# Performance work log

Hardware: AMD Instinct MI355X
Metric: run time of the kernel (lower is better)

## Reference

```python
import jax, jax.numpy as jnp
import numpy as np
from jax.scipy.linalg import solve_triangular

EMB = 2048; NKH = 16; NVH = 32; DK = 128; DV = 128
KSZ = 4; EPS = 1e-6; CHUNK = 64
KEY_DIM = NKH * DK; VAL_DIM = NVH * DV
CONV_DIM = 2 * KEY_DIM + VAL_DIM  # q,k (key_dim each) + v (value_dim)
B, S = 1, 4096  # S % CHUNK == 0 -> no padding path


def setup_inputs() -> dict:
    key = jax.random.key(0)
    ks = jax.random.split(key, 7)
    s = 0.02
    return {
        "hidden_states": jax.random.normal(ks[0], (B, S, EMB), jnp.float32),
        "W_qkvz": jax.random.normal(ks[1], (EMB, 2 * KEY_DIM + 2 * VAL_DIM), jnp.float32) * s,
        "W_ba": jax.random.normal(ks[2], (EMB, 2 * NVH), jnp.float32) * s,
        "conv_kernel": jax.random.normal(ks[3], (KSZ, 1, CONV_DIM), jnp.float32) * 0.1,
        "A_log": jnp.log(jax.random.uniform(ks[4], (NVH,), jnp.float32, 1e-9, 16.0)),
        "dt_bias": jnp.ones((NVH,), jnp.float32),
        "norm_weight": jnp.ones((DV,), jnp.float32),
        "W_out": jax.random.normal(ks[5], (VAL_DIM, EMB), jnp.float32) * s,
    }


def _chunk_gated_delta_rule(q, k, v, g, beta):
    """q,k: [B,S,H,DK]; v: [B,S,H,DV]; g,beta: [B,S,H]. Returns [B,S,H,DV]."""
    dt = q.dtype
    prec = jax.lax.Precision.HIGHEST
    q = jnp.transpose(q, (0, 2, 1, 3)).astype(jnp.float32)
    k = jnp.transpose(k, (0, 2, 1, 3)).astype(jnp.float32)
    v = jnp.transpose(v, (0, 2, 1, 3)).astype(jnp.float32)
    beta = jnp.transpose(beta, (0, 2, 1)).astype(jnp.float32)
    g = jnp.transpose(g, (0, 2, 1)).astype(jnp.float32)
    b, h, s, dk = k.shape
    dv = v.shape[-1]
    nc = s // CHUNK
    q = q * jax.lax.rsqrt(jnp.float32(dk))
    v_beta = v * beta[..., None]
    k_beta = k * beta[..., None]
    qc = q.reshape(b, h, nc, CHUNK, dk)
    kc = k.reshape(b, h, nc, CHUNK, dk)
    kbc = k_beta.reshape(b, h, nc, CHUNK, dk)
    vbc = v_beta.reshape(b, h, nc, CHUNK, dv)
    gc = g.reshape(b, h, nc, CHUNK)
    g_cum = jnp.cumsum(gc, axis=-1)                        # [b,h,nc,C]
    g_diff = g_cum[..., :, None] - g_cum[..., None, :]     # [b,h,nc,C,C]
    decay = jnp.exp(jnp.tril(g_diff))
    tri_incl = jnp.triu(jnp.ones((CHUNK, CHUNK), bool), k=0)
    L = -jnp.matmul(kbc, jnp.swapaxes(kc, -1, -2), precision=prec) * decay
    L = jnp.where(tri_incl, 0.0, L)  # strictly lower
    eye = jnp.eye(CHUNK, dtype=jnp.float32)
    # UT transform: original fori_loop forward-substitution == (I - L)^{-1}
    attn = solve_triangular(eye - L, jnp.broadcast_to(eye, L.shape), lower=True)
    v_intra = jnp.matmul(attn, vbc, precision=prec)
    k_cumdecay = jnp.matmul(attn, kbc * jnp.exp(g_cum)[..., None], precision=prec)
    state0 = jnp.zeros((b, h, dk, dv), jnp.float32)
    tri_strict = jnp.triu(jnp.ones((CHUNK, CHUNK), bool), k=1)
    xs = tuple(jnp.moveaxis(t, 2, 0) for t in (qc, kc, v_intra, k_cumdecay, g_cum, decay))

    def scan_body(state, x):
        q_i, k_i, v_i, kcd_i, g_i, dm_i = x
        a_i = jnp.matmul(q_i, jnp.swapaxes(k_i, -1, -2), precision=prec) * dm_i
        a_i = jnp.where(tri_strict, 0.0, a_i)
        v_new = v_i - jnp.matmul(kcd_i, state, precision=prec)
        out_i = jnp.matmul(q_i * jnp.exp(g_i)[..., None], state, precision=prec) \
              + jnp.matmul(a_i, v_new, precision=prec)
        g_last = g_i[..., -1]
        new_state = state * jnp.exp(g_last)[..., None, None] \
            + jnp.matmul(jnp.swapaxes(k_i * jnp.exp(g_last[..., None] - g_i)[..., None], -1, -2),
                         v_new, precision=prec)
        return new_state, out_i

    _, out = jax.lax.scan(scan_body, state0, xs)
    out = jnp.moveaxis(out, 0, 2).reshape(b, h, s, dv)
    return jnp.transpose(out, (0, 2, 1, 3)).astype(dt)


def reference(hidden_states, W_qkvz, W_ba, conv_kernel, A_log, dt_bias, norm_weight, W_out):
    b, s, _ = hidden_states.shape
    vk = NVH // NKH  # v heads per k head
    qkvz = hidden_states @ W_qkvz                          # [b,s,12288]
    ba = hidden_states @ W_ba                              # [b,s,64]
    mixed = qkvz.reshape(b, s, NKH, 2 * DK + 2 * vk * DV)
    q, k, v_raw, z_raw = jnp.split(mixed, [DK, 2 * DK, 2 * DK + vk * DV], axis=3)
    value = v_raw.reshape(b, s, NVH, DV)
    z = z_raw.reshape(b, s, NVH, DV)
    mixed_ba = ba.reshape(b, s, NKH, 2 * vk)
    b_raw, a_raw = jnp.split(mixed_ba, [vk], axis=3)
    b_gate = b_raw.reshape(b, s, NVH)
    a_gate = a_raw.reshape(b, s, NVH)
    # depthwise causal conv over the concatenated q,k,v channels
    qkv = jnp.concatenate([q.reshape(b, s, -1), k.reshape(b, s, -1), value.reshape(b, s, -1)], axis=-1)
    x = jnp.pad(qkv, ((0, 0), (KSZ - 1, 0), (0, 0)))
    conv = jax.lax.conv_general_dilated(x, conv_kernel, (1,), 'VALID',
                                        dimension_numbers=('NWC', 'WIO', 'NWC'),
                                        feature_group_count=CONV_DIM)
    qkv_c = jax.nn.silu(conv.astype(jnp.float32)).astype(hidden_states.dtype)
    q_c, k_c, v_c = jnp.split(qkv_c, [KEY_DIM, 2 * KEY_DIM], axis=-1)
    query = q_c.reshape(b, s, NKH, DK)
    key = k_c.reshape(b, s, NKH, DK)
    value = v_c.reshape(b, s, NVH, DV)
    beta = jax.nn.sigmoid(b_gate)
    g = (-jnp.exp(A_log.astype(jnp.float32))
         * jax.nn.softplus(a_gate.astype(jnp.float32) + dt_bias.astype(jnp.float32))
         ).astype(hidden_states.dtype)
    query = jnp.repeat(query, vk, axis=2)
    key = jnp.repeat(key, vk, axis=2)
    core = _chunk_gated_delta_rule(query, key, value, g, beta)  # [b,s,NVH,DV]
    # gated RMSNorm (Mamba2-style): gate first, then normalize
    xf = core.astype(jnp.float32) * jax.nn.silu(z.astype(jnp.float32))
    var = jnp.mean(xf * xf, axis=-1, keepdims=True)
    xf = xf * jax.lax.rsqrt(var + EPS) * norm_weight
    out = xf.astype(hidden_states.dtype).reshape(b, s, VAL_DIM)
    return out @ W_out
```

## Files before the change

kernel.cpp:

```cpp
#include <hip/hip_runtime.h>


typedef __attribute__((ext_vector_type(8))) __bf16 bf16x8;
typedef __attribute__((ext_vector_type(4))) float f32x4;
typedef __bf16 bf16_t;

#define MFMA_BF16(A, B, C) __builtin_amdgcn_mfma_f32_16x16x32_bf16((A), (B), (C), 0, 0, 0)

__device__ __forceinline__ void async16(const bf16_t* g, bf16_t* l) {
  __builtin_amdgcn_global_load_lds(
      (const __attribute__((address_space(1))) unsigned*)g,
      (__attribute__((address_space(3))) unsigned*)l, 16, 0, 0);
}

__device__ __forceinline__ bf16_t f2bf(float x) {
  unsigned u = __builtin_bit_cast(unsigned, x);
  unsigned r = u + 0x7fffu + ((u >> 16) & 1u);
  unsigned short s = (unsigned short)(r >> 16);
  return __builtin_bit_cast(bf16_t, s);
}
__device__ __forceinline__ float bf2f(bf16_t b) {
  unsigned short s = __builtin_bit_cast(unsigned short, b);
  unsigned u = ((unsigned)s) << 16;
  return __builtin_bit_cast(float, u);
}
__device__ __forceinline__ unsigned packhl(float x) {
  bf16_t h = f2bf(x);
  bf16_t l = f2bf(x - bf2f(h));
  return (((unsigned)__builtin_bit_cast(unsigned short, h)) << 16) |
         (unsigned)__builtin_bit_cast(unsigned short, l);
}
__device__ __forceinline__ float upk(unsigned u) {
  return __builtin_bit_cast(float, u & 0xffff0000u) +
         __builtin_bit_cast(float, u << 16);
}

struct FragPair { bf16x8 hi, lo; };

__device__ __forceinline__ void load8(float v[8], const float* p) {
  float4 a = *(const float4*)p;
  float4 b = *(const float4*)(p + 4);
  v[0] = a.x; v[1] = a.y; v[2] = a.z; v[3] = a.w;
  v[4] = b.x; v[5] = b.y; v[6] = b.z; v[7] = b.w;
}
__device__ __forceinline__ void load8u(unsigned v[8], const unsigned* p) {
  uint4 a = *(const uint4*)p;
  uint4 b = *(const uint4*)(p + 4);
  v[0] = a.x; v[1] = a.y; v[2] = a.z; v[3] = a.w;
  v[4] = b.x; v[5] = b.y; v[6] = b.z; v[7] = b.w;
}
__device__ __forceinline__ FragPair split8(const float v[8]) {
  FragPair f;
#pragma unroll
  for (int j = 0; j < 8; j++) {
    bf16_t h = f2bf(v[j]);
    f.hi[j] = h;
    f.lo[j] = f2bf(v[j] - bf2f(h));
  }
  return f;
}
__device__ __forceinline__ FragPair unpack8(const unsigned v[8]) {
  FragPair f;
#pragma unroll
  for (int j = 0; j < 8; j++) {
    f.hi[j] = __builtin_bit_cast(bf16_t, (unsigned short)(v[j] >> 16));
    f.lo[j] = __builtin_bit_cast(bf16_t, (unsigned short)(v[j] & 0xffffu));
  }
  return f;
}
__device__ __forceinline__ f32x4 mfma3(const FragPair& A, const FragPair& B, f32x4 c) {
  c = MFMA_BF16(A.hi, B.hi, c);
  c = MFMA_BF16(A.hi, B.lo, c);
  c = MFMA_BF16(A.lo, B.hi, c);
  return c;
}

__global__ void k_cvt(const float* __restrict__ in, bf16_t* __restrict__ out, int n) {
  int i = (blockIdx.x * 256 + threadIdx.x) * 4;
  if (i + 3 < n) {
    float4 v = *(const float4*)(in + i);
    out[i + 0] = f2bf(v.x); out[i + 1] = f2bf(v.y);
    out[i + 2] = f2bf(v.z); out[i + 3] = f2bf(v.w);
  }
}

__global__ void k_transpose_cvt(const float* __restrict__ in, bf16_t* __restrict__ out,
                                int K, int N) {
  __shared__ bf16_t tile[64 * 65];
  int n0 = blockIdx.x * 64, k0 = blockIdx.y * 64;
  int c = threadIdx.x & 63, rg = threadIdx.x >> 6;
#pragma unroll
  for (int rr = 0; rr < 16; rr++) {
    int r = rr * 4 + rg;
    tile[c * 65 + r] = f2bf(in[(size_t)(k0 + r) * N + n0 + c]);
  }
  __syncthreads();
#pragma unroll
  for (int rr = 0; rr < 16; rr++) {
    int r = rr * 4 + rg;
    out[(size_t)(n0 + r) * K + k0 + c] = tile[r * 65 + c];
  }
}

__global__ void k_ktrans(const bf16_t* __restrict__ kb, bf16_t* __restrict__ kbT) {
  __shared__ __align__(16) bf16_t t[128][72];
  int kh = blockIdx.x >> 6, ci = blockIdx.x & 63, s0 = ci * 64;
  int s = threadIdx.x & 63, dg = threadIdx.x >> 6;
  const bf16_t* src = kb + (size_t)(s0 + s) * 2048 + kh * 128 + dg * 32;
#pragma unroll
  for (int j = 0; j < 4; j++) {
    bf16x8 v = *(const bf16x8*)(src + j * 8);
#pragma unroll
    for (int e = 0; e < 8; e++) t[dg * 32 + j * 8 + e][s] = v[e];
  }
  __syncthreads();
  int d = threadIdx.x >> 1, sh = (threadIdx.x & 1) * 32;
  bf16_t* dst = kbT + ((size_t)blockIdx.x * 128 + d) * 64 + sh;
#pragma unroll
  for (int j = 0; j < 4; j++)
    *(bf16x8*)(dst + j * 8) = *(const bf16x8*)(&t[d][sh + j * 8]);
}

__global__ __launch_bounds__(256) void k_gemm(const bf16_t* __restrict__ A,
                                              const bf16_t* __restrict__ BT,
                                              float* __restrict__ C, int M, int N, int K) {
  __shared__ __align__(16) bf16_t sA[128 * 32];
  __shared__ __align__(16) bf16_t sB[128 * 32];
  const int tid = threadIdx.x;
  const int lane = tid & 63, w = tid >> 6;
  const int quad = lane >> 4, l15 = lane & 15;
  const int m0 = blockIdx.y * 128, n0 = blockIdx.x * 128;
  const int wm = (w >> 1) * 64, wn = (w & 1) * 64;
  f32x4 acc[4][4];
#pragma unroll
  for (int a = 0; a < 4; a++)
#pragma unroll
    for (int b = 0; b < 4; b++) { f32x4 z = {0.f, 0.f, 0.f, 0.f}; acc[a][b] = z; }
  const int sb = (lane & 7) ^ ((lane >> 3) & 7);
  const int srow = ((tid >> 3) << 1) + (sb >> 2);
  const int scol = (sb & 3) * 8;
  const bf16_t* gA = A + (size_t)(m0 + srow) * K + scol;
  const bf16_t* gB = BT + (size_t)(n0 + srow) * K + scol;
  bf16_t* lA = sA + w * 512;
  bf16_t* lB = sB + w * 512;
  const int rh = l15 >> 1;
  const int bs = (((l15 & 1) << 2) + quad) ^ rh;
  const int foff = rh * 64 + bs * 8;
  for (int kt = 0; kt < K; kt += 32) {
    async16(gA + kt, lA);
    async16(gA + (size_t)64 * K + kt, lA + 2048);
    async16(gB + kt, lB);
    async16(gB + (size_t)64 * K + kt, lB + 2048);
    __syncthreads();
    bf16x8 af[4], bfv[4];
#pragma unroll
    for (int t = 0; t < 4; t++) {
      af[t]  = *(const bf16x8*)(sA + ((wm >> 1) + t * 8) * 64 + foff);
      bfv[t] = *(const bf16x8*)(sB + ((wn >> 1) + t * 8) * 64 + foff);
    }
#pragma unroll
    for (int mt = 0; mt < 4; mt++)
#pragma unroll
      for (int nt = 0; nt < 4; nt++)
        acc[mt][nt] = MFMA_BF16(af[mt], bfv[nt], acc[mt][nt]);
    __syncthreads();
  }
#pragma unroll
  for (int mt = 0; mt < 4; mt++)
#pragma unroll
    for (int nt = 0; nt < 4; nt++) {
      int row0 = m0 + wm + mt * 16 + quad * 4;
      int col = n0 + wn + nt * 16 + l15;
#pragma unroll
      for (int r = 0; r < 4; r++)
        C[(size_t)(row0 + r) * N + col] = acc[mt][nt][r];
    }
}

__global__ __launch_bounds__(256) void k_gemm_qkvz(const bf16_t* __restrict__ A,
                                                   const bf16_t* __restrict__ BT,
                                                   bf16_t* __restrict__ qkvb,
                                                   bf16_t* __restrict__ zb,
                                                   int M, int N, int K) {
  __shared__ __align__(16) bf16_t sA[128 * 32];
  __shared__ __align__(16) bf16_t sB[128 * 32];
  const int tid = threadIdx.x;
  const int lane = tid & 63, w = tid >> 6;
  const int quad = lane >> 4, l15 = lane & 15;
  const int m0 = blockIdx.y * 128, n0 = blockIdx.x * 128;
  const int wm = (w >> 1) * 64, wn = (w & 1) * 64;
  f32x4 acc[4][4];
#pragma unroll
  for (int a = 0; a < 4; a++)
#pragma unroll
    for (int b = 0; b < 4; b++) { f32x4 z = {0.f, 0.f, 0.f, 0.f}; acc[a][b] = z; }
  const int sb = (lane & 7) ^ ((lane >> 3) & 7);
  const int srow = ((tid >> 3) << 1) + (sb >> 2);
  const int scol = (sb & 3) * 8;
  const bf16_t* gA = A + (size_t)(m0 + srow) * K + scol;
  const bf16_t* gB = BT + (size_t)(n0 + srow) * K + scol;
  bf16_t* lA = sA + w * 512;
  bf16_t* lB = sB + w * 512;
  const int rh = l15 >> 1;
  const int bs = (((l15 & 1) << 2) + quad) ^ rh;
  const int foff = rh * 64 + bs * 8;
  for (int kt = 0; kt < K; kt += 32) {
    async16(gA + kt, lA);
    async16(gA + (size_t)64 * K + kt, lA + 2048);
    async16(gB + kt, lB);
    async16(gB + (size_t)64 * K + kt, lB + 2048);
    __syncthreads();
    bf16x8 af[4], bfv[4];
#pragma unroll
    for (int t = 0; t < 4; t++) {
      af[t]  = *(const bf16x8*)(sA + ((wm >> 1) + t * 8) * 64 + foff);
      bfv[t] = *(const bf16x8*)(sB + ((wn >> 1) + t * 8) * 64 + foff);
    }
#pragma unroll
    for (int mt = 0; mt < 4; mt++)
#pragma unroll
      for (int nt = 0; nt < 4; nt++)
        acc[mt][nt] = MFMA_BF16(af[mt], bfv[nt], acc[mt][nt]);
    __syncthreads();
  }
#pragma unroll
  for (int nt = 0; nt < 4; nt++) {
    int c = n0 + wn + nt * 16 + l15;
    int kh = c / 768;
    int rr = c - kh * 768;
    bool isz = (rr >= 512);
    bf16_t* dst = isz ? zb : qkvb;
    size_t stride = isz ? 4096 : 8192;
    size_t coff = isz ? (size_t)(kh * 256 + (rr - 512)) : (size_t)(kh * 512 + rr);
#pragma unroll
    for (int mt = 0; mt < 4; mt++) {
      int row0 = m0 + wm + mt * 16 + quad * 4;
#pragma unroll
      for (int r = 0; r < 4; r++)
        dst[(size_t)(row0 + r) * stride + coff] = f2bf(acc[mt][nt][r]);
    }
  }
}

__global__ __launch_bounds__(256) void k_ba(const float* __restrict__ hs,
                                            const float* __restrict__ Wba,
                                            const float* __restrict__ A_log,
                                            const float* __restrict__ dtb,
                                            float* __restrict__ g, float* __restrict__ beta) {
  __shared__ float sH[4][2048];
  int s0 = blockIdx.x * 32;
  int c = threadIdx.x & 63, sg = threadIdx.x >> 6;
  for (int rg = 0; rg < 8; rg++) {
    __syncthreads();
    for (int i = threadIdx.x; i < 2048; i += 256) {
      int r = i >> 9, kk = (i & 511) * 4;
      *(float4*)(&sH[r][kk]) = *(const float4*)(hs + (size_t)(s0 + rg * 4 + r) * 2048 + kk);
    }
    __syncthreads();
    float dot = 0.f;
    for (int kk = 0; kk < 2048; kk += 4) {
      float4 hv = *(const float4*)(&sH[sg][kk]);
      dot += hv.x * Wba[(kk + 0) * 64 + c] + hv.y * Wba[(kk + 1) * 64 + c] +
             hv.z * Wba[(kk + 2) * 64 + c] + hv.w * Wba[(kk + 3) * 64 + c];
    }
    int s = s0 + rg * 4 + sg;
    int hh = c >> 2, j = c & 3;
    if (j < 2) {
      int vh = hh * 2 + j;
      beta[s * 32 + vh] = 1.f / (1.f + __expf(-dot));
    } else {
      int vh = hh * 2 + (j - 2);
      float x = dot + dtb[vh];
      float sp = (x > 20.f) ? x : log1pf(__expf(x));
      g[s * 32 + vh] = -__expf(A_log[vh]) * sp;
    }
  }
}

__global__ void k_conv(const bf16_t* __restrict__ qkvb, const float* __restrict__ ck,
                       bf16_t* __restrict__ qb, bf16_t* __restrict__ kb,
                       bf16_t* __restrict__ vb) {
  int c = blockIdx.x * 256 + threadIdx.x;
  int s0 = blockIdx.y * 128;
  int col, dstc, dstride;
  bf16_t* dst;
  float scale = 1.0f;
  if (c < 2048) {
    int hh = c >> 7, d = c & 127;
    col = hh * 512 + d; dst = qb; dstc = c; dstride = 2048;
    scale = 0.08838834764831845f;
  } else if (c < 4096) {
    int cc = c - 2048, hh = cc >> 7, d = cc & 127;
    col = hh * 512 + 128 + d; dst = kb; dstc = cc; dstride = 2048;
  } else {
    int cc = c - 4096, vh = cc >> 7, d = cc & 127;
    col = (vh >> 1) * 512 + 256 + (vh & 1) * 128 + d; dst = vb; dstc = cc; dstride = 4096;
  }
  float w0 = ck[c], w1 = ck[8192 + c], w2 = ck[2 * 8192 + c], w3 = ck[3 * 8192 + c];
  float x0 = 0.f, x1 = 0.f, x2 = 0.f;
  if (s0 >= 3) {
    x0 = bf2f(qkvb[(size_t)(s0 - 3) * 8192 + col]);
    x1 = bf2f(qkvb[(size_t)(s0 - 2) * 8192 + col]);
    x2 = bf2f(qkvb[(size_t)(s0 - 1) * 8192 + col]);
  }
  for (int s = s0; s < s0 + 128; s++) {
    float x3 = bf2f(qkvb[(size_t)s * 8192 + col]);
    float y = w0 * x0 + w1 * x1 + w2 * x2 + w3 * x3;
    y = y / (1.f + __expf(-y));
    dst[(size_t)s * dstride + dstc] = f2bf(y * scale);
    x0 = x1; x1 = x2; x2 = x3;
  }
}

__global__ __launch_bounds__(256) void k_phaseA(const bf16_t* __restrict__ kb,
                                                const bf16_t* __restrict__ vb,
                                                const float* __restrict__ g,
                                                const float* __restrict__ beta,
                                                float* __restrict__ vi,
                                                bf16_t* __restrict__ kcdn) {
  __shared__ __align__(16) char smem[36608];
  float* sGc = (float*)smem;
  float* sBt = (float*)(smem + 256);
  float* sBE = (float*)(smem + 512);
  float* sP  = (float*)(smem + 768);
  bf16_t* sQ  = (bf16_t*)(smem + 18176);
  bf16_t* sQT = (bf16_t*)(smem + 27392);
  bf16_t* sVT = (bf16_t*)(smem + 18176);
  bf16_t* sKT = (bf16_t*)(smem + 27392);

  const int tid = threadIdx.x, lane = tid & 63, w = tid >> 6;
  const int quad = lane >> 4, l15 = lane & 15;
  const int h = blockIdx.x >> 6, ci = blockIdx.x & 63;
  const int kh = h >> 1, s0 = ci * 64;
  const int m = w * 16 + l15;

  if (tid < 64) {
    float gv = g[(size_t)(s0 + tid) * 32 + h];
    float bv = beta[(size_t)(s0 + tid) * 32 + h];
#pragma unroll
    for (int off = 1; off < 64; off <<= 1) {
      float t = __shfl_up(gv, off, 64);
      if (tid >= off) gv += t;
    }
    sGc[tid] = gv; sBt[tid] = bv; sBE[tid] = bv * __expf(gv);
  }
  __syncthreads();

  const bf16_t* krow = kb + (size_t)s0 * 2048 + kh * 128;
  bf16x8 ak[4];
#pragma unroll
  for (int ks = 0; ks < 4; ks++)
    ak[ks] = *(const bf16x8*)(krow + (size_t)m * 2048 + ks * 32 + quad * 8);
  f32x4 accL[4];
#pragma unroll
  for (int nt = 0; nt < 4; nt++) { f32x4 z = {0.f, 0.f, 0.f, 0.f}; accL[nt] = z; }
#pragma unroll
  for (int nt = 0; nt < 4; nt++)
#pragma unroll
    for (int ks = 0; ks < 4; ks++) {
      bf16x8 bk = *(const bf16x8*)(krow + (size_t)(nt * 16 + l15) * 2048 + ks * 32 + quad * 8);
      accL[nt] = MFMA_BF16(ak[ks], bk, accL[nt]);
    }
#pragma unroll
  for (int nt = 0; nt < 4; nt++) {
    int j = nt * 16 + l15;
#pragma unroll
    for (int r = 0; r < 4; r++) {
      int i = w * 16 + quad * 4 + r;
      float Lij = (i > j) ? (-accL[nt][r] * sBt[i] * __expf(sGc[i] - sGc[j])) : 0.f;
      sP[i * 68 + j] = ((i == j) ? 1.f : 0.f) + Lij;
      bf16_t q16 = f2bf(Lij);
      sQ[i * 72 + j] = q16;
      sQT[j * 72 + i] = q16;
    }
  }
  __syncthreads();

  for (int it = 0; it < 5; it++) {
    f32x4 accQ[4];
#pragma unroll
    for (int nt = 0; nt < 4; nt++) { f32x4 z = {0.f, 0.f, 0.f, 0.f}; accQ[nt] = z; }
    bf16x8 qa[2];
#pragma unroll
    for (int ks = 0; ks < 2; ks++)
      qa[ks] = *(const bf16x8*)(sQ + m * 72 + ks * 32 + quad * 8);
#pragma unroll
    for (int nt = 0; nt < 4; nt++)
#pragma unroll
      for (int ks = 0; ks < 2; ks++) {
        bf16x8 qv = *(const bf16x8*)(sQT + (nt * 16 + l15) * 72 + ks * 32 + quad * 8);
        accQ[nt] = MFMA_BF16(qa[ks], qv, accQ[nt]);
      }
    __syncthreads();
#pragma unroll
    for (int nt = 0; nt < 4; nt++) {
      int j = nt * 16 + l15;
#pragma unroll
      for (int r = 0; r < 4; r++) {
        int i = w * 16 + quad * 4 + r;
        bf16_t q16 = f2bf(accQ[nt][r]);
        sQ[i * 72 + j] = q16;
        sQT[j * 72 + i] = q16;
      }
    }
    __syncthreads();
    f32x4 accP[4];
#pragma unroll
    for (int nt = 0; nt < 4; nt++) { f32x4 z = {0.f, 0.f, 0.f, 0.f}; accP[nt] = z; }
    FragPair pa[2];
#pragma unroll
    for (int ks = 0; ks < 2; ks++) {
      float v[8];
      load8(v, sP + m * 68 + ks * 32 + quad * 8);
      pa[ks] = split8(v);
    }
#pragma unroll
    for (int nt = 0; nt < 4; nt++)
#pragma unroll
      for (int ks = 0; ks < 2; ks++) {
        bf16x8 qv = *(const bf16x8*)(sQT + (nt * 16 + l15) * 72 + ks * 32 + quad * 8);
        accP[nt] = MFMA_BF16(pa[ks].hi, qv, accP[nt]);
        accP[nt] = MFMA_BF16(pa[ks].lo, qv, accP[nt]);
      }
#pragma unroll
    for (int nt = 0; nt < 4; nt++) {
      int j = nt * 16 + l15;
#pragma unroll
      for (int r = 0; r < 4; r++) {
        int i = w * 16 + quad * 4 + r;
        sP[i * 68 + j] += accP[nt][r];
      }
    }
  }

  FragPair paV[2], paK[2];
#pragma unroll
  for (int ks = 0; ks < 2; ks++) {
    float v[8];
    load8(v, sP + m * 68 + ks * 32 + quad * 8);
    float vv[8], vk[8];
#pragma unroll
    for (int jj = 0; jj < 8; jj++) {
      int i = ks * 32 + quad * 8 + jj;
      vv[jj] = v[jj] * sBt[i];
      vk[jj] = v[jj] * sBE[i];
    }
    paV[ks] = split8(vv);
    paK[ks] = split8(vk);
  }

  for (int hf = 0; hf < 2; hf++) {
    __syncthreads();
    {
      int sidx = tid & 63, dg = tid >> 6;
      const bf16_t* vsrc = vb + (size_t)(s0 + sidx) * 4096 + h * 128 + hf * 64 + dg * 16;
      const bf16_t* ksrc = kb + (size_t)(s0 + sidx) * 2048 + kh * 128 + hf * 64 + dg * 16;
      bf16x8 v0 = *(const bf16x8*)vsrc;
      bf16x8 v1 = *(const bf16x8*)(vsrc + 8);
      bf16x8 k0 = *(const bf16x8*)ksrc;
      bf16x8 k1 = *(const bf16x8*)(ksrc + 8);
#pragma unroll
      for (int e = 0; e < 8; e++) {
        sVT[(dg * 16 + e) * 72 + sidx] = v0[e];
        sVT[(dg * 16 + 8 + e) * 72 + sidx] = v1[e];
        sKT[(dg * 16 + e) * 72 + sidx] = k0[e];
        sKT[(dg * 16 + 8 + e) * 72 + sidx] = k1[e];
      }
    }
    __syncthreads();
    f32x4 accV[4], accK[4];
#pragma unroll
    for (int nt = 0; nt < 4; nt++) {
      f32x4 z = {0.f, 0.f, 0.f, 0.f};
      accV[nt] = z; accK[nt] = z;
    }
#pragma unroll
    for (int nt = 0; nt < 4; nt++)
#pragma unroll
      for (int ks = 0; ks < 2; ks++) {
        bf16x8 bv = *(const bf16x8*)(sVT + (nt * 16 + l15) * 72 + ks * 32 + quad * 8);
        accV[nt] = MFMA_BF16(paV[ks].hi, bv, accV[nt]);
        accV[nt] = MFMA_BF16(paV[ks].lo, bv, accV[nt]);
        bf16x8 bk = *(const bf16x8*)(sKT + (nt * 16 + l15) * 72 + ks * 32 + quad * 8);
        accK[nt] = MFMA_BF16(paK[ks].hi, bk, accK[nt]);
        accK[nt] = MFMA_BF16(paK[ks].lo, bk, accK[nt]);
      }
#pragma unroll
    for (int nt = 0; nt < 4; nt++) {
      int col = hf * 64 + nt * 16 + l15;
#pragma unroll
      for (int r = 0; r < 4; r++) {
        int row = w * 16 + quad * 4 + r;
        size_t o = ((size_t)h * 4096 + s0 + row) * 128 + col;
        vi[o] = accV[nt][r];
        kcdn[o] = f2bf(-accK[nt][r]);
      }
    }
  }
}

__global__ __launch_bounds__(256) void k_phaseB(const bf16_t* __restrict__ qb,
                                                const bf16_t* __restrict__ kbT,
                                                const float* __restrict__ g,
                                                const float* __restrict__ vi,
                                                const bf16_t* __restrict__ kcdn,
                                                bf16_t* __restrict__ vnT,
                                                bf16_t* __restrict__ outp) {
  __shared__ __align__(16) char smem[13312];
  float* sGc2 = (float*)smem;
  unsigned* sSTp = (unsigned*)(smem + 512);
  unsigned* sVTp = (unsigned*)(smem + 8960);
  const int tid = threadIdx.x, lane = tid & 63, w = tid >> 6;
  const int quad = lane >> 4, l15 = lane & 15;
  const int h = blockIdx.x >> 3, cg = blockIdx.x & 7;
  const int kh = h >> 1, col0 = cg * 16;
  const int m = w * 16 + l15;

  for (int i = tid; i < 16 * 132; i += 256) sSTp[i] = 0u;
  if (tid < 64) {
    float gv = g[(size_t)tid * 32 + h];
#pragma unroll
    for (int off = 1; off < 64; off <<= 1) {
      float t = __shfl_up(gv, off, 64);
      if (tid >= off) gv += t;
    }
    sGc2[tid] = gv;
  }
  __syncthreads();

  for (int ci = 0; ci < 64; ci++) {
    const int s0 = ci * 64;
    const float* sGc = sGc2 + (ci & 1) * 64;

    const bf16_t* kcrow = kcdn + ((size_t)h * 4096 + s0 + m) * 128;
    const bf16_t* qrow = qb + (size_t)(s0 + m) * 2048 + kh * 128;
    bf16x8 a1[4], a2[4], kT[2][2];
#pragma unroll
    for (int d = 0; d < 4; d++) {
      a1[d] = *(const bf16x8*)(kcrow + d * 32 + quad * 8);
      a2[d] = *(const bf16x8*)(qrow + d * 32 + quad * 8);
    }
#pragma unroll
    for (int mi = 0; mi < 2; mi++)
#pragma unroll
      for (int ks = 0; ks < 2; ks++)
        kT[mi][ks] = *(const bf16x8*)(kbT + ((size_t)(kh * 64 + ci) * 128 +
                                             w * 32 + mi * 16 + l15) * 64 + ks * 32 + quad * 8);
    const int colg = col0 + l15;
    size_t vbase = ((size_t)h * 4096 + s0 + w * 16 + quad * 4) * 128 + colg;
    f32x4 accV = {vi[vbase], vi[vbase + 128], vi[vbase + 256], vi[vbase + 384]};
    f32x4 accO = {0.f, 0.f, 0.f, 0.f};
#pragma unroll
    for (int d = 0; d < 4; d++) {
      unsigned u[8];
      load8u(u, sSTp + l15 * 132 + d * 32 + quad * 8);
      FragPair B = unpack8(u);
      accV = MFMA_BF16(a1[d], B.hi, accV);
      accV = MFMA_BF16(a1[d], B.lo, accV);
      accO = MFMA_BF16(a2[d], B.hi, accO);
      accO = MFMA_BF16(a2[d], B.lo, accO);
    }
    const float gl = sGc[63];
    {
      bf16_t* vout = vnT + ((size_t)(h * 64 + ci) * 128 + colg) * 64 + w * 16 + quad * 4;
      bf16_t* oout = outp + vbase;
      ushort4 vv;
      unsigned pk[4];
      unsigned short vb_[4];
#pragma unroll
      for (int r = 0; r < 4; r++) {
        float gr = sGc[w * 16 + quad * 4 + r];
        oout[(size_t)r * 128] = f2bf(accO[r] * __expf(gr));
        vb_[r] = __builtin_bit_cast(unsigned short, f2bf(accV[r]));
        pk[r] = packhl(accV[r] * __expf(gl - gr));
      }
      vv.x = vb_[0]; vv.y = vb_[1]; vv.z = vb_[2]; vv.w = vb_[3];
      *(ushort4*)vout = vv;
      uint4 pv; pv.x = pk[0]; pv.y = pk[1]; pv.z = pk[2]; pv.w = pk[3];
      *(uint4*)(sVTp + l15 * 68 + w * 16 + quad * 4) = pv;
    }
    __syncthreads();

    f32x4 accD[2];
#pragma unroll
    for (int mi = 0; mi < 2; mi++) { f32x4 z = {0.f, 0.f, 0.f, 0.f}; accD[mi] = z; }
#pragma unroll
    for (int ks = 0; ks < 2; ks++) {
      unsigned u[8];
      load8u(u, sVTp + l15 * 68 + ks * 32 + quad * 8);
      FragPair Bv = unpack8(u);
#pragma unroll
      for (int mi = 0; mi < 2; mi++) {
        accD[mi] = MFMA_BF16(kT[mi][ks], Bv.hi, accD[mi]);
        accD[mi] = MFMA_BF16(kT[mi][ks], Bv.lo, accD[mi]);
      }
    }
    float egl = __expf(gl);
#pragma unroll
    for (int mi = 0; mi < 2; mi++) {
      int row0 = w * 32 + mi * 16 + quad * 4;
      unsigned* ps = sSTp + l15 * 132 + row0;
      uint4 old4 = *(uint4*)ps;
      uint4 nu;
      nu.x = packhl(upk(old4.x) * egl + accD[mi][0]);
      nu.y = packhl(upk(old4.y) * egl + accD[mi][1]);
      nu.z = packhl(upk(old4.z) * egl + accD[mi][2]);
      nu.w = packhl(upk(old4.w) * egl + accD[mi][3]);
      *(uint4*)ps = nu;
    }
    if (ci + 1 < 64 && tid < 64) {
      float gv = g[(size_t)((ci + 1) * 64 + tid) * 32 + h];
#pragma unroll
      for (int off = 1; off < 64; off <<= 1) {
        float t = __shfl_up(gv, off, 64);
        if (tid >= off) gv += t;
      }
      sGc2[((ci + 1) & 1) * 64 + tid] = gv;
    }
    __syncthreads();
  }
}

__global__ __launch_bounds__(256) void k_phaseC(const bf16_t* __restrict__ qb,
                                                const bf16_t* __restrict__ kb,
                                                const float* __restrict__ g,
                                                const bf16_t* __restrict__ vnT,
                                                const bf16_t* __restrict__ outp,
                                                const bf16_t* __restrict__ zb,
                                                const float* __restrict__ nw,
                                                bf16_t* __restrict__ xf) {
  __shared__ __align__(16) char smem[17664];
  float* sGc = (float*)smem;
  unsigned* sAp = (unsigned*)(smem + 256);
  const int tid = threadIdx.x, lane = tid & 63, w = tid >> 6;
  const int quad = lane >> 4, l15 = lane & 15;
  const int h = blockIdx.x >> 6, ci = blockIdx.x & 63;
  const int kh = h >> 1, s0 = ci * 64;
  const int m = w * 16 + l15;

  if (tid < 64) {
    float gv = g[(size_t)(s0 + tid) * 32 + h];
#pragma unroll
    for (int off = 1; off < 64; off <<= 1) {
      float t = __shfl_up(gv, off, 64);
      if (tid >= off) gv += t;
    }
    sGc[tid] = gv;
  }
  __syncthreads();

  const bf16_t* qrow = qb + (size_t)s0 * 2048 + kh * 128;
  const bf16_t* krow = kb + (size_t)s0 * 2048 + kh * 128;
  bf16x8 aq[4];
#pragma unroll
  for (int ks = 0; ks < 4; ks++)
    aq[ks] = *(const bf16x8*)(qrow + (size_t)m * 2048 + ks * 32 + quad * 8);
  f32x4 accA[4];
#pragma unroll
  for (int nt = 0; nt < 4; nt++) { f32x4 z = {0.f, 0.f, 0.f, 0.f}; accA[nt] = z; }
#pragma unroll
  for (int nt = 0; nt < 4; nt++)
#pragma unroll
    for (int ks = 0; ks < 4; ks++) {
      bf16x8 bk = *(const bf16x8*)(krow + (size_t)(nt * 16 + l15) * 2048 + ks * 32 + quad * 8);
      accA[nt] = MFMA_BF16(aq[ks], bk, accA[nt]);
    }
#pragma unroll
  for (int nt = 0; nt < 4; nt++) {
    int j = nt * 16 + l15;
#pragma unroll
    for (int r = 0; r < 4; r++) {
      int i = w * 16 + quad * 4 + r;
      float a = (i >= j) ? accA[nt][r] * __expf(sGc[i] - sGc[j]) : 0.f;
      sAp[i * 68 + j] = packhl(a);
    }
  }
  __syncthreads();

  FragPair Aa[2];
#pragma unroll
  for (int ks = 0; ks < 2; ks++) {
    unsigned u[8];
    load8u(u, sAp + m * 68 + ks * 32 + quad * 8);
    Aa[ks] = unpack8(u);
  }
  f32x4 accO[8];
#pragma unroll
  for (int nt = 0; nt < 8; nt++) {
    size_t base = ((size_t)h * 4096 + s0 + w * 16 + quad * 4) * 128 + nt * 16 + l15;
    f32x4 z;
    z[0] = bf2f(outp[base]); z[1] = bf2f(outp[base + 128]);
    z[2] = bf2f(outp[base + 256]); z[3] = bf2f(outp[base + 384]);
    accO[nt] = z;
  }
#pragma unroll
  for (int nt = 0; nt < 8; nt++)
#pragma unroll
    for (int ks = 0; ks < 2; ks++) {
      bf16x8 bv = *(const bf16x8*)(vnT + ((size_t)(h * 64 + ci) * 128 + nt * 16 + l15) * 64 +
                                   ks * 32 + quad * 8);
      accO[nt] = MFMA_BF16(Aa[ks].hi, bv, accO[nt]);
      accO[nt] = MFMA_BF16(Aa[ks].lo, bv, accO[nt]);
    }

  float xv[8][4];
  float ss[4] = {0.f, 0.f, 0.f, 0.f};
#pragma unroll
  for (int nt = 0; nt < 8; nt++) {
    int dv = nt * 16 + l15;
#pragma unroll
    for (int r = 0; r < 4; r++) {
      int s = s0 + w * 16 + quad * 4 + r;
      float z = bf2f(zb[(size_t)s * 4096 + h * 128 + dv]);
      float gate = z / (1.f + __expf(-z));
      float val = accO[nt][r] * gate;
      xv[nt][r] = val;
      ss[r] += val * val;
    }
  }
#pragma unroll
  for (int off = 1; off < 16; off <<= 1) {
#pragma unroll
    for (int r = 0; r < 4; r++) ss[r] += __shfl_xor(ss[r], off, 64);
  }
  float rs[4];
#pragma unroll
  for (int r = 0; r < 4; r++) rs[r] = rsqrtf(ss[r] * (1.f / 128.f) + 1e-6f);
#pragma unroll
  for (int nt = 0; nt < 8; nt++) {
    int dv = nt * 16 + l15;
    float nwv = nw[dv];
#pragma unroll
    for (int r = 0; r < 4; r++) {
      int s = s0 + w * 16 + quad * 4 + r;
      xf[(size_t)s * 4096 + h * 128 + dv] = f2bf(xv[nt][r] * rs[r] * nwv);
    }
  }
}

extern "C" void kernel_launch(void* const* d_in, const int* in_sizes, int n_in,
                              void* d_out, int out_size, void* d_ws, size_t ws_size,
                              hipStream_t stream) {
  const float* hs = (const float*)d_in[0];
  const float* Wqkvz = (const float*)d_in[1];
  const float* Wba = (const float*)d_in[2];
  const float* convk = (const float*)d_in[3];
  const float* A_log = (const float*)d_in[4];
  const float* dtb = (const float*)d_in[5];
  const float* nw = (const float*)d_in[6];
  const float* Wout = (const float*)d_in[7];
  float* out = (float*)d_out;
  char* ws = (char*)d_ws;

  const size_t NEED = 252706816u;
  if (ws_size < NEED) return;

  bf16_t* hsbf = (bf16_t*)(ws + 0);
  bf16_t* wqkT = (bf16_t*)(ws + 16777216);
  bf16_t* qb   = (bf16_t*)(ws + 0);
  bf16_t* kb   = (bf16_t*)(ws + 16777216);
  bf16_t* vb   = (bf16_t*)(ws + 33554432);
  bf16_t* vnT  = (bf16_t*)(ws + 33554432);
  bf16_t* qkvb = (bf16_t*)(ws + 67108864);
  float*  vi   = (float*)(ws + 67108864);
  bf16_t* xf   = (bf16_t*)(ws + 67108864);
  bf16_t* zb   = (bf16_t*)(ws + 134217728);
  float*  gbuf = (float*)(ws + 167772160);
  float*  bbuf = (float*)(ws + 168296448);
  bf16_t* kcdn = (bf16_t*)(ws + 168820736);
  bf16_t* woutT= (bf16_t*)(ws + 168820736);
  bf16_t* outp = (bf16_t*)(ws + 202375168);
  bf16_t* kbT  = (bf16_t*)(ws + 235929600);

  k_cvt<<<8192, 256, 0, stream>>>(hs, hsbf, 4096 * 2048);
  k_transpose_cvt<<<dim3(192, 32), 256, 0, stream>>>(Wqkvz, wqkT, 2048, 12288);
  k_gemm_qkvz<<<dim3(96, 32), 256, 0, stream>>>(hsbf, wqkT, qkvb, zb,
                                                4096, 12288, 2048);
  k_ba<<<128, 256, 0, stream>>>(hs, Wba, A_log, dtb, gbuf, bbuf);
  k_conv<<<dim3(32, 32), 256, 0, stream>>>(qkvb, convk, qb, kb, vb);
  k_ktrans<<<1024, 256, 0, stream>>>(kb, kbT);
  k_phaseA<<<2048, 256, 0, stream>>>(kb, vb, gbuf, bbuf, vi, kcdn);
  k_phaseB<<<256, 256, 0, stream>>>(qb, kbT, gbuf, vi, kcdn, vnT, outp);
  k_phaseC<<<2048, 256, 0, stream>>>(qb, kb, gbuf, vnT, outp, zb, nw, xf);
  k_transpose_cvt<<<dim3(32, 64), 256, 0, stream>>>(Wout, woutT, 4096, 2048);
  k_gemm<<<dim3(16, 32), 256, 0, stream>>>(xf, woutT, out, 4096, 2048, 4096);
}
```

Before: 1.096 ms.

## Rewrite QKVZ GEMM with 256x256 tiles, 4-stage async LDS pipeline, XCD swizzle

After: 1.094 ms. About the same (-0.2%).

```diff
diff --git a/kernel.cpp b/kernel.cpp
--- a/kernel.cpp
+++ b/kernel.cpp
@@ -67,12 +67,6 @@
     f.lo[j] = __builtin_bit_cast(bf16_t, (unsigned short)(v[j] & 0xffffu));
   }
   return f;
-}
-__device__ __forceinline__ f32x4 mfma3(const FragPair& A, const FragPair& B, f32x4 c) {
-  c = MFMA_BF16(A.hi, B.hi, c);
-  c = MFMA_BF16(A.hi, B.lo, c);
-  c = MFMA_BF16(A.lo, B.hi, c);
-  return c;
 }
 
 __global__ void k_cvt(const float* __restrict__ in, bf16_t* __restrict__ out, int n) {
@@ -177,55 +171,93 @@
     }
 }
 
-__global__ __launch_bounds__(256) void k_gemm_qkvz(const bf16_t* __restrict__ A,
-                                                   const bf16_t* __restrict__ BT,
-                                                   bf16_t* __restrict__ qkvb,
-                                                   bf16_t* __restrict__ zb,
-                                                   int M, int N, int K) {
-  __shared__ __align__(16) bf16_t sA[128 * 32];
-  __shared__ __align__(16) bf16_t sB[128 * 32];
+__global__ __launch_bounds__(512, 2) void k_gemm_qkvz(const bf16_t* __restrict__ A,
+                                                      const bf16_t* __restrict__ BT,
+                                                      bf16_t* __restrict__ qkvb,
+                                                      bf16_t* __restrict__ zb,
+                                                      int M, int N, int K) {
+  __shared__ __align__(16) bf16_t sA[4 * 8192];
+  __shared__ __align__(16) bf16_t sB[4 * 8192];
   const int tid = threadIdx.x;
   const int lane = tid & 63, w = tid >> 6;
   const int quad = lane >> 4, l15 = lane & 15;
-  const int m0 = blockIdx.y * 128, n0 = blockIdx.x * 128;
-  const int wm = (w >> 1) * 64, wn = (w & 1) * 64;
-  f32x4 acc[4][4];
-#pragma unroll
-  for (int a = 0; a < 4; a++)
-#pragma unroll
-    for (int b = 0; b < 4; b++) { f32x4 z = {0.f, 0.f, 0.f, 0.f}; acc[a][b] = z; }
-  const int sb = (lane & 7) ^ ((lane >> 3) & 7);
-  const int srow = ((tid >> 3) << 1) + (sb >> 2);
-  const int scol = (sb & 3) * 8;
-  const bf16_t* gA = A + (size_t)(m0 + srow) * K + scol;
-  const bf16_t* gB = BT + (size_t)(n0 + srow) * K + scol;
-  bf16_t* lA = sA + w * 512;
-  bf16_t* lB = sB + w * 512;
-  const int rh = l15 >> 1;
-  const int bs = (((l15 & 1) << 2) + quad) ^ rh;
-  const int foff = rh * 64 + bs * 8;
-  for (int kt = 0; kt < K; kt += 32) {
-    async16(gA + kt, lA);
-    async16(gA + (size_t)64 * K + kt, lA + 2048);
-    async16(gB + kt, lB);
-    async16(gB + (size_t)64 * K + kt, lB + 2048);
-    __syncthreads();
-    bf16x8 af[4], bfv[4];
-#pragma unroll
-    for (int t = 0; t < 4; t++) {
-      af[t]  = *(const bf16x8*)(sA + ((wm >> 1) + t * 8) * 64 + foff);
-      bfv[t] = *(const bf16x8*)(sB + ((wn >> 1) + t * 8) * 64 + foff);
-    }
-#pragma unroll
-    for (int mt = 0; mt < 4; mt++)
-#pragma unroll
-      for (int nt = 0; nt < 4; nt++)
-        acc[mt][nt] = MFMA_BF16(af[mt], bfv[nt], acc[mt][nt]);
-    __syncthreads();
-  }
-#pragma unroll
-  for (int nt = 0; nt < 4; nt++) {
-    int c = n0 + wn + nt * 16 + l15;
+
+  const int nwg = gridDim.x * gridDim.y;
+  const int cpx = nwg >> 3;
+  int id = blockIdx.y * gridDim.x + blockIdx.x;
+  id = (id & 7) * cpx + (id >> 3);
+  const int bx = id % gridDim.x, by = id / gridDim.x;
+  const int m0 = by * 256, n0 = bx * 256;
+  const int wm = (w >> 2) * 128, wn = (w & 3) * 64;
+
+  f32x4 acc[8][4];
+#pragma unroll
+  for (int m = 0; m < 8; m++)
+#pragma unroll
+    for (int n = 0; n < 4; n++) { f32x4 z = {0.f, 0.f, 0.f, 0.f}; acc[m][n] = z; }
+
+  const int srow = w * 16 + (lane >> 2);
+  const int sq = (lane & 3) ^ ((lane >> 3) & 3);
+  const bf16_t* gA = A + (size_t)(m0 + srow) * K + sq * 8;
+  const bf16_t* gB = BT + (size_t)(n0 + srow) * K + sq * 8;
+  const size_t rowskip = (size_t)128 * K;
+
+  const int pblk = (quad ^ ((l15 >> 1) & 3)) << 3;
+  const int fA = (wm + l15) * 32 + pblk;
+  const int fB = (wn + l15) * 32 + pblk;
+
+  const int NT = K >> 5;
+
+  auto stage = [&](int t) {
+    bf16_t* lA = sA + (t & 3) * 8192 + w * 512;
+    bf16_t* lB = sB + (t & 3) * 8192 + w * 512;
+    const bf16_t* pA = gA + t * 32;
+    const bf16_t* pB = gB + t * 32;
+    async16(pA, lA);
+    async16(pA + rowskip, lA + 4096);
+    async16(pB, lB);
+    async16(pB + rowskip, lB + 4096);
+  };
+
+  if (0 < NT) stage(0);
+  if (1 < NT) stage(1);
+  if (2 < NT) stage(2);
+
+  for (int t = 0; t < NT; ++t) {
+    if (t + 3 < NT) stage(t + 3);
+    const int ahead = NT - 1 - t;
+    if (ahead >= 3)      asm volatile("s_waitcnt vmcnt(12)" ::: "memory");
+    else if (ahead == 2) asm volatile("s_waitcnt vmcnt(8)" ::: "memory");
+    else if (ahead == 1) asm volatile("s_waitcnt vmcnt(4)" ::: "memory");
+    else                 asm volatile("s_waitcnt vmcnt(0)" ::: "memory");
+    __builtin_amdgcn_s_barrier();
+    asm volatile("" ::: "memory");
+    __builtin_amdgcn_sched_barrier(0);
+
+    const bf16_t* bA = sA + (t & 3) * 8192;
+    const bf16_t* bB = sB + (t & 3) * 8192;
+    bf16x8 af[8], bfv[4];
+#pragma unroll
+    for (int m = 0; m < 8; m++) af[m] = *(const bf16x8*)(bA + fA + m * 512);
+#pragma unroll
+    for (int n = 0; n < 4; n++) bfv[n] = *(const bf16x8*)(bB + fB + n * 512);
+
+    __builtin_amdgcn_s_setprio(1);
+#pragma unroll
+    for (int m = 0; m < 8; m++)
+#pragma unroll
+      for (int n = 0; n < 4; n++)
+        acc[m][n] = MFMA_BF16(af[m], bfv[n], acc[m][n]);
+    __builtin_amdgcn_s_setprio(0);
+
+    asm volatile("" ::: "memory");
+    __builtin_amdgcn_sched_barrier(0);
+    __builtin_amdgcn_s_barrier();
+  }
+
+#pragma unroll
+  for (int n = 0; n < 4; n++) {
+    int c = n0 + wn + n * 16 + l15;
     int kh = c / 768;
     int rr = c - kh * 768;
     bool isz = (rr >= 512);
@@ -233,11 +265,11 @@
     size_t stride = isz ? 4096 : 8192;
     size_t coff = isz ? (size_t)(kh * 256 + (rr - 512)) : (size_t)(kh * 512 + rr);
 #pragma unroll
-    for (int mt = 0; mt < 4; mt++) {
-      int row0 = m0 + wm + mt * 16 + quad * 4;
+    for (int m = 0; m < 8; m++) {
+      int row0 = m0 + wm + m * 16 + quad * 4;
 #pragma unroll
       for (int r = 0; r < 4; r++)
-        dst[(size_t)(row0 + r) * stride + coff] = f2bf(acc[mt][nt][r]);
+        dst[(size_t)(row0 + r) * stride + coff] = f2bf(acc[m][n][r]);
     }
   }
 }
@@ -774,7 +806,7 @@
 
   k_cvt<<<8192, 256, 0, stream>>>(hs, hsbf, 4096 * 2048);
   k_transpose_cvt<<<dim3(192, 32), 256, 0, stream>>>(Wqkvz, wqkT, 2048, 12288);
-  k_gemm_qkvz<<<dim3(96, 32), 256, 0, stream>>>(hsbf, wqkT, qkvb, zb,
+  k_gemm_qkvz<<<dim3(48, 16), 512, 0, stream>>>(hsbf, wqkT, qkvb, zb,
                                                 4096, 12288, 2048);
   k_ba<<<128, 256, 0, stream>>>(hs, Wba, A_log, dtb, gbuf, bbuf);
   k_conv<<<dim3(32, 32), 256, 0, stream>>>(qkvb, convk, qb, kb, vb);
```
